# Kernel tuning notes

Measured on AMD Instinct MI355X. Metric: run time of the kernel, lower is better.

The kernel has to match this reference:

```python
import jax, jax.numpy as jnp
import numpy as np

N, M = 50000, 12
ORIG, NBR_F, AF = 92, 41, 64
B, NA = 500, 100
NCONV = 3
BN_EPS = 1e-5


def _batchnorm(x, g, b):
    # training-mode batchnorm over axis 0 (biased variance, like torch)
    mu = jnp.mean(x, axis=0)
    var = jnp.mean((x - mu) ** 2, axis=0)
    return (x - mu) * jax.lax.rsqrt(var + BN_EPS) * g + b


def _conv_layer(atom, nbr_fea, nbr_idx, W, bW, g1, b1, g2, b2):
    n, m = nbr_idx.shape
    atom_nbr = atom[nbr_idx]                                   # [N,M,AF] gather
    center = jnp.broadcast_to(atom[:, None, :], (n, m, AF))
    total = jnp.concatenate([center, atom_nbr, nbr_fea], axis=2)  # [N,M,2AF+NBR_F]
    gated = jnp.einsum('nmf,of->nmo', total, W) + bW              # [N,M,2AF]
    gated = _batchnorm(gated.reshape(-1, 2 * AF), g1, b1).reshape(n, m, 2 * AF)
    filt, core = gated[..., :AF], gated[..., AF:]
    summed = jnp.sum(jax.nn.sigmoid(filt) * jax.nn.softplus(core), axis=1)  # [N,AF]
    summed = _batchnorm(summed, g2, b2)
    return jax.nn.softplus(atom + summed)


def setup_inputs() -> dict:
    key = jax.random.key(0)
    ks = jax.random.split(key, 12)
    inp = {
        'atom_fea': jax.random.normal(ks[0], (N, ORIG), jnp.float32),
        'nbr_fea': jax.random.normal(ks[1], (N, M, NBR_F), jnp.float32),
        'nbr_fea_idx': jax.random.randint(ks[2], (N, M), 0, N, jnp.int32),
        'crystal_atom_idx': jnp.arange(B * NA, dtype=jnp.int32).reshape(B, NA),
        'mask': jnp.ones((ORIG,), jnp.float32),
        'emb_W': jax.random.normal(ks[3], (AF, ORIG), jnp.float32) * 0.05,
        'conv_W': jax.random.normal(ks[4], (NCONV, 2 * AF, 2 * AF + NBR_F), jnp.float32) * 0.05,
        'conv_b': jnp.zeros((NCONV, 2 * AF), jnp.float32),
        'bn1_g': jnp.ones((NCONV, 2 * AF), jnp.float32),
        'bn1_b': jnp.zeros((NCONV, 2 * AF), jnp.float32),
        'bn2_g': jnp.ones((NCONV, AF), jnp.float32),
        'bn2_b': jnp.zeros((NCONV, AF), jnp.float32),
        'fc1_W': jax.random.normal(ks[5], (AF, AF), jnp.float32) * 0.05,
        'fc1_b': jnp.zeros((AF,), jnp.float32),
        'fc2_W': jax.random.normal(ks[6], (AF, AF), jnp.float32) * 0.05,
        'fc2_b': jnp.zeros((AF,), jnp.float32),
        'out_W': jax.random.normal(ks[7], (1, AF), jnp.float32) * 0.05,
        'out_b': jnp.zeros((1,), jnp.float32),
    }
    return inp


def reference(atom_fea, nbr_fea, nbr_fea_idx, crystal_atom_idx, mask, emb_W,
              conv_W, conv_b, bn1_g, bn1_b, bn2_g, bn2_b,
              fc1_W, fc1_b, fc2_W, fc2_b, out_W, out_b):
    x = atom_fea * mask                      # learned input mask
    atom_mask_feature = x
    h = x @ emb_W.T                          # embedding, no bias -> [N,AF]
    for i in range(NCONV):
        h = _conv_layer(h, nbr_fea, nbr_fea_idx, conv_W[i], conv_b[i],
                        bn1_g[i], bn1_b[i], bn2_g[i], bn2_b[i])
    g = h[crystal_atom_idx]                  # [B,NA,AF]
    norm = jnp.sqrt(jnp.sum(g * g, axis=-1, keepdims=True))
    g = g / jnp.maximum(norm, 1e-12)         # F.normalize p=2
    pooled = jnp.mean(g, axis=1)             # [B,AF]
    z = jax.nn.softplus(pooled @ fc1_W.T + fc1_b)
    z = jax.nn.softplus(z @ fc2_W.T + fc2_b)
    props = z @ out_W.T + out_b              # [B,1]
    return props, atom_mask_feature
```

## Files before the change

kernel.cpp:

```cpp
#include <hip/hip_runtime.h>
#include <hip/hip_bf16.h>
#include <stdint.h>

#define NN      50000
#define MMN     12
#define NMROWS  600000
#define ORIGF   92
#define NBRF    41
#define AFD     64
#define GCH     128
#define KTOT    169
#define BBC     500
#define NAA     100
#define BN_EPS  1e-5f
#define GROWS   96

typedef unsigned short u16;
typedef __attribute__((ext_vector_type(8))) short bf16x8;
typedef __attribute__((ext_vector_type(4))) float f32x4;
typedef __attribute__((ext_vector_type(4))) unsigned int u32x4;

__device__ __forceinline__ float b2f(u16 u) {
    union { uint32_t i; float f; } v; v.i = ((uint32_t)u) << 16; return v.f;
}
__device__ __forceinline__ float hi2f(uint32_t p) {
    union { uint32_t i; float f; } v; v.i = p & 0xffff0000u; return v.f;
}
__device__ __forceinline__ u16 f2b(float f) {
    __hip_bfloat16 h = __float2bfloat16(f);
    return *(u16*)&h;
}
__device__ __forceinline__ float sp_f(float x) {
    return fmaxf(x, 0.f) + __logf(1.f + __expf(-fabsf(x)));
}
__device__ __forceinline__ float sigm_f(float x) {
    return __builtin_amdgcn_rcpf(1.f + __expf(-x));
}

__global__ void k_mask(const float* __restrict__ atom, const float* __restrict__ mask,
                       float* __restrict__ dout) {
    int i = blockIdx.x * blockDim.x + threadIdx.x;
    int stride = gridDim.x * blockDim.x;
    for (; i < NN * ORIGF; i += stride) {
        int k = i % ORIGF;
        dout[BBC + i] = atom[i] * mask[k];
    }
}

__global__ __launch_bounds__(256, 2) void k_emb(const float* __restrict__ atom,
                                                const float* __restrict__ mask,
                                                const float* __restrict__ embW,
                                                u16* __restrict__ h) {
    __shared__ float xs[4 * 96];
    int lane = threadIdx.x & 63;
    int w = threadIdx.x >> 6;
    float wr[ORIGF];
#pragma unroll
    for (int k = 0; k < ORIGF; ++k) wr[k] = embW[lane * ORIGF + k];
    float m1 = mask[lane];
    float m2 = (lane < ORIGF - 64) ? mask[64 + lane] : 0.f;
    for (int base = blockIdx.x * 4; base < NN; base += gridDim.x * 4) {
        int n = base + w;
        xs[w * 96 + lane] = atom[(size_t)n * ORIGF + lane] * m1;
        if (lane < ORIGF - 64)
            xs[w * 96 + 64 + lane] = atom[(size_t)n * ORIGF + 64 + lane] * m2;
        __syncthreads();
        float acc = 0.f;
#pragma unroll
        for (int k4 = 0; k4 < ORIGF / 4; ++k4) {
            float4 f = *(const float4*)&xs[w * 96 + 4 * k4];
            acc += f.x * wr[4*k4] + f.y * wr[4*k4+1] + f.z * wr[4*k4+2] + f.w * wr[4*k4+3];
        }
        h[(size_t)n * AFD + lane] = f2b(acc);
        __syncthreads();
    }
}

__global__ __launch_bounds__(256, 2) void k_cn(const u16* __restrict__ h,
                                               const float* __restrict__ convW,
                                               uint32_t* __restrict__ C32) {
    __shared__ float xs[2 * AFD];
    int lane = threadIdx.x & 63;
    int w = threadIdx.x >> 6;
    int half = w & 1;
    int sub = w >> 1;
    int koff = half * AFD;
    float wa[AFD], wb[AFD];
#pragma unroll
    for (int k = 0; k < AFD; ++k) {
        wa[k] = convW[lane * KTOT + koff + k];
        wb[k] = convW[(lane + 64) * KTOT + koff + k];
    }
    for (int base = blockIdx.x * 2; base < NN; base += gridDim.x * 2) {
        int n = base + sub;
        if (half == 0) xs[sub * AFD + lane] = b2f(h[(size_t)n * AFD + lane]);
        __syncthreads();
        float aa = 0.f, ab = 0.f;
#pragma unroll
        for (int k4 = 0; k4 < AFD / 4; ++k4) {
            float4 f = *(const float4*)&xs[sub * AFD + 4 * k4];
            aa += f.x * wa[4*k4] + f.y * wa[4*k4+1] + f.z * wa[4*k4+2] + f.w * wa[4*k4+3];
            ab += f.x * wb[4*k4] + f.y * wb[4*k4+1] + f.z * wb[4*k4+2] + f.w * wb[4*k4+3];
        }
        C32[(size_t)n * 128 + half * 64 + lane] = (uint32_t)f2b(aa) | ((uint32_t)f2b(ab) << 16);
        __syncthreads();
    }
}

__device__ __forceinline__ void stage_nbrf(const float* nbrf, int r0, float* fs) {
    const float4* src = (const float4*)(nbrf + (size_t)r0 * NBRF);
    for (int t = threadIdx.x; t < (GROWS * NBRF) / 4; t += 256) {
        float4 f = src[t];
        float vals[4] = {f.x, f.y, f.z, f.w};
#pragma unroll
        for (int j = 0; j < 4; ++j) {
            int e = t * 4 + j;
            int row = e / NBRF;
            int k = e - row * NBRF;
            fs[row * 44 + k] = vals[j];
        }
    }
}

template<bool STORE>
__global__ __launch_bounds__(256, 4) void k_gs5(
    const uint32_t* __restrict__ C32, const float* __restrict__ nbrf,
    const int* __restrict__ nbridx, const float* __restrict__ convW,
    const float* __restrict__ convb, float* __restrict__ stats,
    uint32_t* __restrict__ gated32)
{
    __shared__ __align__(16) u16 As[GROWS * 48];
    __shared__ __align__(16) uint32_t C2T[64 * 100];
    __shared__ __align__(16) uint32_t C1T[64 * 12];
    const int tid  = threadIdx.x;
    const int lane = tid & 63;
    const int w    = tid >> 6;
    const int lr   = lane & 15;
    const int lg   = lane >> 4;
    const int r0    = blockIdx.x * GROWS;
    const int nbase = blockIdx.x * (GROWS / MMN);
    const int rowb  = w * 24;

    int jv = nbridx[r0 + rowb + (lane < 24 ? lane : 0)];
    uint32_t c1v[2];
#pragma unroll
    for (int q = 0; q < 2; ++q) {
        int e = tid + q * 256;
        c1v[q] = C32[(size_t)(nbase + (e >> 6)) * 128 + (e & 63)];
    }
    const float4* src4 = (const float4*)(nbrf + (size_t)r0 * NBRF);
    float4 af[4];
#pragma unroll
    for (int it = 0; it < 4; ++it) {
        int t = tid + it * 256;
        if (it < 3 || t < 984) af[it] = src4[t];
    }
    const int chlo = w * 16 + lr;
    const int chhi = chlo + 64;
    const float* wlo = convW + (size_t)chlo * KTOT + 128;
    const float* whi = convW + (size_t)chhi * KTOT + 128;
    bf16x8 bl0, bh0;
    bf16x8 bl1 = {0,0,0,0,0,0,0,0}, bh1 = {0,0,0,0,0,0,0,0};
#pragma unroll
    for (int e = 0; e < 8; ++e) {
        bl0[e] = (short)f2b(wlo[8 * lg + e]);
        bh0[e] = (short)f2b(whi[8 * lg + e]);
    }
    if (lg == 0) {
#pragma unroll
        for (int e = 0; e < 8; ++e) {
            bl1[e] = (short)f2b(wlo[32 + e]);
            bh1[e] = (short)f2b(whi[32 + e]);
        }
    } else if (lg == 1) {
        bl1[0] = (short)f2b(wlo[40]); bl1[1] = (short)f2b(convb[chlo]);
        bh1[0] = (short)f2b(whi[40]); bh1[1] = (short)f2b(convb[chhi]);
    }
    uint32_t c2v[24];
#pragma unroll
    for (int rr = 0; rr < 24; ++rr) {
        int j = __shfl(jv, rr, 64);
        c2v[rr] = C32[(size_t)j * 128 + 64 + lane];
    }
#pragma unroll
    for (int it = 0; it < 4; ++it) {
        int t = tid + it * 256;
        if (it < 3 || t < 984) {
            float4 f = af[it];
            float vals[4] = {f.x, f.y, f.z, f.w};
#pragma unroll
            for (int jj = 0; jj < 4; ++jj) {
                int e = t * 4 + jj;
                int row = e / NBRF;
                int k = e - row * NBRF;
                As[row * 48 + k] = f2b(vals[jj]);
            }
        }
    }
    for (int e = tid; e < 672; e += 256) {
        int row = e / 7;
        int k = 41 + (e - row * 7);
        As[row * 48 + k] = (k == 41) ? (u16)0x3F80 : (u16)0;
    }
#pragma unroll
    for (int q = 0; q < 2; ++q) {
        int e = tid + q * 256;
        C1T[(e & 63) * 12 + (e >> 6)] = c1v[q];
    }
#pragma unroll
    for (int rr = 0; rr < 24; ++rr) C2T[lane * 100 + rowb + rr] = c2v[rr];
    __syncthreads();

    f32x4 acc[6][2];
    const f32x4 z = {0.f, 0.f, 0.f, 0.f};
    const bf16x8 zb = {0,0,0,0,0,0,0,0};
#pragma unroll
    for (int mt = 0; mt < 6; ++mt) {
        const u16* ap = &As[(mt * 16 + lr) * 48 + 8 * lg];
        bf16x8 a0 = *(const bf16x8*)ap;
        bf16x8 a1 = zb;
        if (lg < 2) a1 = *(const bf16x8*)(ap + 32);
        acc[mt][0] = __builtin_amdgcn_mfma_f32_16x16x32_bf16(a1, bl1,
                     __builtin_amdgcn_mfma_f32_16x16x32_bf16(a0, bl0, z, 0, 0, 0), 0, 0, 0);
        acc[mt][1] = __builtin_amdgcn_mfma_f32_16x16x32_bf16(a1, bh1,
                     __builtin_amdgcn_mfma_f32_16x16x32_bf16(a0, bh0, z, 0, 0, 0), 0, 0, 0);
    }

    const int word = w * 16 + lr;
    float slo = 0.f, qlo = 0.f, shi = 0.f, qhi = 0.f;
#pragma unroll
    for (int mt = 0; mt < 6; ++mt) {
        u32x4 p2 = *(const u32x4*)&C2T[word * 100 + mt * 16 + 4 * lg];
#pragma unroll
        for (int rg = 0; rg < 4; ++rg) {
            int row = mt * 16 + 4 * lg + rg;
            uint32_t p1 = C1T[word * 12 + row / MMN];
            float glo = acc[mt][0][rg] + b2f((u16)p1) + b2f((u16)p2[rg]);
            float ghi = acc[mt][1][rg] + hi2f(p1) + hi2f(p2[rg]);
            if (STORE) {
                gated32[(size_t)(r0 + row) * 64 + word] =
                    (uint32_t)f2b(glo) | ((uint32_t)f2b(ghi) << 16);
            }
            slo += glo; qlo = fmaf(glo, glo, qlo);
            shi += ghi; qhi = fmaf(ghi, ghi, qhi);
        }
    }
    slo += __shfl_xor(slo, 16, 64); slo += __shfl_xor(slo, 32, 64);
    qlo += __shfl_xor(qlo, 16, 64); qlo += __shfl_xor(qlo, 32, 64);
    shi += __shfl_xor(shi, 16, 64); shi += __shfl_xor(shi, 32, 64);
    qhi += __shfl_xor(qhi, 16, 64); qhi += __shfl_xor(qhi, 32, 64);
    if (lane < 16) {
        atomicAdd(&stats[word], slo);
        atomicAdd(&stats[128 + word], qlo);
        atomicAdd(&stats[64 + word], shi);
        atomicAdd(&stats[128 + 64 + word], qhi);
    }
}

__global__ void k_fin(float* __restrict__ stats, const float* __restrict__ gg,
                      const float* __restrict__ bb, int nch, float invcnt,
                      int sumoff, int sqoff, int scoff, int shoff) {
    int c = threadIdx.x;
    if (c < nch) {
        float mean = stats[sumoff + c] * invcnt;
        float var  = fmaxf(stats[sqoff + c] * invcnt - mean * mean, 0.f);
        float sc   = gg[c] * rsqrtf(var + BN_EPS);
        stats[scoff + c] = sc;
        stats[shoff + c] = bb[c] - mean * sc;
    }
}

__global__ __launch_bounds__(256) void k_acts(
    const uint32_t* __restrict__ gated32, float* __restrict__ stats,
    u16* __restrict__ summed)
{
    __shared__ float red[4][64][2];
    int lane = threadIdx.x & 63;
    int w = threadIdx.x >> 6;
    float sa = stats[384 + lane],      ba = stats[512 + lane];
    float sb = stats[384 + 64 + lane], bb = stats[512 + 64 + lane];
    int wave = blockIdx.x * 4 + w, nw = gridDim.x * 4;
    float s2 = 0.f, q2 = 0.f;
    for (int n = wave; n < NN; n += nw) {
        const uint32_t* gr = gated32 + (size_t)n * MMN * 64;
        float s = 0.f;
#pragma unroll
        for (int m = 0; m < MMN; ++m) {
            uint32_t p = gr[m * 64 + lane];
            float f1 = b2f((u16)p) * sa + ba;
            float cc = hi2f(p) * sb + bb;
            s += sigm_f(f1) * sp_f(cc);
        }
        summed[(size_t)n * AFD + lane] = f2b(s);
        s2 += s; q2 += s * s;
    }
    red[w][lane][0] = s2; red[w][lane][1] = q2;
    __syncthreads();
    if (threadIdx.x < 64) {
        int c = threadIdx.x;
        float a = 0, b = 0;
#pragma unroll
        for (int ww = 0; ww < 4; ++ww) { a += red[ww][c][0]; b += red[ww][c][1]; }
        atomicAdd(&stats[256 + c], a);
        atomicAdd(&stats[320 + c], b);
    }
}

__device__ __forceinline__ void edge_dot(const float* fr, const float* wfa,
                                         const float* wfb, float& aa, float& ab) {
#pragma unroll
    for (int k4 = 0; k4 < 10; ++k4) {
        float4 f = *(const float4*)&fr[4 * k4];
        aa += f.x * wfa[4*k4] + f.y * wfa[4*k4+1] + f.z * wfa[4*k4+2] + f.w * wfa[4*k4+3];
        ab += f.x * wfb[4*k4] + f.y * wfb[4*k4+1] + f.z * wfb[4*k4+2] + f.w * wfb[4*k4+3];
    }
    aa += fr[40] * wfa[40];
    ab += fr[40] * wfb[40];
}

__global__ __launch_bounds__(256) void k_act(
    const uint32_t* __restrict__ C32, const float* __restrict__ nbrf,
    const int* __restrict__ nbridx, const float* __restrict__ convW,
    const float* __restrict__ convb, float* __restrict__ stats,
    u16* __restrict__ summed)
{
    __shared__ float fs[GROWS * 44];
    __shared__ float red[4][64][2];
    int lane = threadIdx.x & 63;
    int w = threadIdx.x >> 6;
    int r0 = blockIdx.x * GROWS;
    stage_nbrf(nbrf, r0, fs);
    float wfa[NBRF], wfb[NBRF];
#pragma unroll
    for (int k = 0; k < NBRF; ++k) {
        wfa[k] = convW[lane * KTOT + 128 + k];
        wfb[k] = convW[(lane + 64) * KTOT + 128 + k];
    }
    float biasa = convb[lane], biasb = convb[64 + lane];
    float sa = stats[384 + lane],      ba = stats[512 + lane];
    float sb = stats[384 + 64 + lane], bb = stats[512 + 64 + lane];
    __syncthreads();
    float s2 = 0.f, q2 = 0.f;
    float s = 0.f;
    float c1a = 0.f, c1b = 0.f;
    for (int rr = 0; rr < 24; ++rr) {
        int rl = w * 24 + rr;
        int r = r0 + rl;
        if ((rr % MMN) == 0) {
            int n = r / MMN;
            uint32_t p1 = C32[(size_t)n * 128 + lane];
            c1a = b2f((u16)p1); c1b = b2f((u16)(p1 >> 16));
            s = 0.f;
        }
        int j = nbridx[r];
        uint32_t p2 = C32[(size_t)j * 128 + 64 + lane];
        float aa = c1a + b2f((u16)p2) + biasa;
        float ab = c1b + b2f((u16)(p2 >> 16)) + biasb;
        edge_dot(&fs[rl * 44], wfa, wfb, aa, ab);
        float f1 = aa * sa + ba;
        float cc = ab * sb + bb;
        s += sigm_f(f1) * sp_f(cc);
        if ((rr % MMN) == MMN - 1) {
            int n = r / MMN;
            summed[(size_t)n * AFD + lane] = f2b(s);
            s2 += s; q2 += s * s;
        }
    }
    red[w][lane][0] = s2; red[w][lane][1] = q2;
    __syncthreads();
    if (threadIdx.x < 64) {
        int c = threadIdx.x;
        float a = 0, b = 0;
#pragma unroll
        for (int ww = 0; ww < 4; ++ww) { a += red[ww][c][0]; b += red[ww][c][1]; }
        atomicAdd(&stats[256 + c], a);
        atomicAdd(&stats[320 + c], b);
    }
}

__global__ void k_update(u16* __restrict__ h, const u16* __restrict__ summed,
                         const float* __restrict__ stats) {
    int i = blockIdx.x * blockDim.x + threadIdx.x;
    int st = gridDim.x * blockDim.x;
    int c = threadIdx.x & 63;
    float sc = stats[640 + c], shf = stats[704 + c];
    for (; i < NN * AFD; i += st) {
        float x = b2f(h[i]) + b2f(summed[i]) * sc + shf;
        h[i] = f2b(sp_f(x));
    }
}

__global__ __launch_bounds__(256) void k_pool(const u16* __restrict__ h,
                                              const int* __restrict__ cry,
                                              float* __restrict__ pooled) {
    __shared__ float red[4][64];
    int lane = threadIdx.x & 63, w = threadIdx.x >> 6;
    int b = blockIdx.x;
    float acc = 0.f;
    for (int a = w; a < NAA; a += 4) {
        int idx = cry[b * NAA + a];
        float v = b2f(h[(size_t)idx * AFD + lane]);
        float s2 = v * v;
#pragma unroll
        for (int o = 32; o > 0; o >>= 1) s2 += __shfl_xor(s2, o, 64);
        acc += v / fmaxf(sqrtf(s2), 1e-12f);
    }
    red[w][lane] = acc;
    __syncthreads();
    if (threadIdx.x < 64) {
        float s = red[0][threadIdx.x] + red[1][threadIdx.x] +
                  red[2][threadIdx.x] + red[3][threadIdx.x];
        pooled[b * AFD + threadIdx.x] = s * (1.f / NAA);
    }
}

__global__ __launch_bounds__(64) void k_head(const float* __restrict__ pooled,
    const float* __restrict__ fc1W, const float* __restrict__ fc1b,
    const float* __restrict__ fc2W, const float* __restrict__ fc2b,
    const float* __restrict__ outW, const float* __restrict__ outb,
    float* __restrict__ props) {
    __shared__ float W1[64 * 65], W2[64 * 65], zbuf[64], pbuf[64];
    int l = threadIdx.x;
    for (int e = l; e < 64 * 64; e += 64) {
        int o = e >> 6, k = e & 63;
        W1[o * 65 + k] = fc1W[e];
        W2[o * 65 + k] = fc2W[e];
    }
    int b = blockIdx.x;
    pbuf[l] = pooled[b * AFD + l];
    __syncthreads();
    float acc = fc1b[l];
#pragma unroll
    for (int k = 0; k < 64; ++k) acc += pbuf[k] * W1[l * 65 + k];
    zbuf[l] = sp_f(acc);
    __syncthreads();
    acc = fc2b[l];
#pragma unroll
    for (int k = 0; k < 64; ++k) acc += zbuf[k] * W2[l * 65 + k];
    float v = sp_f(acc) * outW[l];
#pragma unroll
    for (int o = 32; o > 0; o >>= 1) v += __shfl_xor(v, o, 64);
    if (l == 0) props[b] = v + outb[0];
}

extern "C" void kernel_launch(void* const* d_in, const int* in_sizes, int n_in,
                              void* d_out, int out_size, void* d_ws, size_t ws_size,
                              hipStream_t stream) {
    const float* atom  = (const float*)d_in[0];
    const float* nbrf  = (const float*)d_in[1];
    const int* nbridx  = (const int*)d_in[2];
    const int* cry     = (const int*)d_in[3];
    const float* mask  = (const float*)d_in[4];
    const float* embW  = (const float*)d_in[5];
    const float* convW = (const float*)d_in[6];
    const float* convb = (const float*)d_in[7];
    const float* bn1g  = (const float*)d_in[8];
    const float* bn1b  = (const float*)d_in[9];
    const float* bn2g  = (const float*)d_in[10];
    const float* bn2b  = (const float*)d_in[11];
    const float* fc1W  = (const float*)d_in[12];
    const float* fc1b  = (const float*)d_in[13];
    const float* fc2W  = (const float*)d_in[14];
    const float* fc2b  = (const float*)d_in[15];
    const float* outW  = (const float*)d_in[16];
    const float* outb  = (const float*)d_in[17];

    char* ws = (char*)d_ws;
    float* stats    = (float*)ws;
    float* pooled   = (float*)(ws + 4096);
    u16*   h        = (u16*)(ws + (1u << 20));
    u16*   summed   = (u16*)(ws + (8u << 20));
    uint32_t* C32   = (uint32_t*)(ws + (16u << 20));
    uint32_t* gated32 = (uint32_t*)(ws + (48u << 20));
    const bool bigws = ws_size >= (size_t)(48u << 20) + 153600000u;

    float* out_props = (float*)d_out;

    k_mask<<<2048, 256, 0, stream>>>(atom, mask, (float*)d_out);
    k_emb<<<512, 256, 0, stream>>>(atom, mask, embW, h);
    for (int i = 0; i < 3; ++i) {
        hipMemsetAsync(stats, 0, 384 * sizeof(float), stream);
        k_cn<<<1024, 256, 0, stream>>>(h, convW + (size_t)i * GCH * KTOT, C32);
        if (bigws)
            k_gs5<true><<<NMROWS / GROWS, 256, 0, stream>>>(C32, nbrf, nbridx,
                convW + (size_t)i * GCH * KTOT, convb + (size_t)i * GCH, stats, gated32);
        else
            k_gs5<false><<<NMROWS / GROWS, 256, 0, stream>>>(C32, nbrf, nbridx,
                convW + (size_t)i * GCH * KTOT, convb + (size_t)i * GCH, stats, gated32);
        k_fin<<<1, 128, 0, stream>>>(stats, bn1g + (size_t)i * GCH, bn1b + (size_t)i * GCH,
                                     128, 1.f / NMROWS, 0, 128, 384, 512);
        if (bigws)
            k_acts<<<1024, 256, 0, stream>>>(gated32, stats, summed);
        else
            k_act<<<NMROWS / GROWS, 256, 0, stream>>>(C32, nbrf, nbridx,
                convW + (size_t)i * GCH * KTOT, convb + (size_t)i * GCH, stats, summed);
        k_fin<<<1, 128, 0, stream>>>(stats, bn2g + (size_t)i * AFD, bn2b + (size_t)i * AFD,
                                     64, 1.f / NN, 256, 320, 640, 704);
        k_update<<<1024, 256, 0, stream>>>(h, summed, stats);
    }
    k_pool<<<BBC, 256, 0, stream>>>(h, cry, pooled);
    k_head<<<BBC, 64, 0, stream>>>(pooled, fc1W, fc1b, fc2W, fc2b, outW, outb, out_props);
}
```

Baseline: 1.041 ms.

## Recompute gated tile in a second MFMA pass instead of storing gated buffer

Replaces the stats pass plus the separate activation kernel with one templated kernel run twice. The first pass only accumulates batchnorm statistics. The second recomputes the gated values with MFMA and applies sigmoid·softplus, reducing per-atom sums in shared memory. This drops the large gated32 write and read-back in exchange for redoing the gather and matmul. The neighbor gathers now go straight to LDS via global_load_lds, replacing register staging and the transposed LDS writes.

```diff
diff --git a/kernel.cpp b/kernel.cpp
--- a/kernel.cpp
+++ b/kernel.cpp
@@ -18,7 +18,6 @@
 typedef unsigned short u16;
 typedef __attribute__((ext_vector_type(8))) short bf16x8;
 typedef __attribute__((ext_vector_type(4))) float f32x4;
-typedef __attribute__((ext_vector_type(4))) unsigned int u32x4;
 
 __device__ __forceinline__ float b2f(u16 u) {
     union { uint32_t i; float f; } v; v.i = ((uint32_t)u) << 16; return v.f;
@@ -35,6 +34,11 @@
 }
 __device__ __forceinline__ float sigm_f(float x) {
     return __builtin_amdgcn_rcpf(1.f + __expf(-x));
+}
+__device__ __forceinline__ void gll4(const void* g, void* l) {
+    __builtin_amdgcn_global_load_lds(
+        (const __attribute__((address_space(1))) void*)g,
+        (__attribute__((address_space(3))) void*)l, 4, 0, 0);
 }
 
 __global__ void k_mask(const float* __restrict__ atom, const float* __restrict__ mask,
@@ -107,46 +111,37 @@
     }
 }
 
-__device__ __forceinline__ void stage_nbrf(const float* nbrf, int r0, float* fs) {
-    const float4* src = (const float4*)(nbrf + (size_t)r0 * NBRF);
-    for (int t = threadIdx.x; t < (GROWS * NBRF) / 4; t += 256) {
-        float4 f = src[t];
-        float vals[4] = {f.x, f.y, f.z, f.w};
-#pragma unroll
-        for (int j = 0; j < 4; ++j) {
-            int e = t * 4 + j;
-            int row = e / NBRF;
-            int k = e - row * NBRF;
-            fs[row * 44 + k] = vals[j];
-        }
-    }
-}
-
-template<bool STORE>
-__global__ __launch_bounds__(256, 4) void k_gs5(
+template<int PASS>
+__global__ __launch_bounds__(256, 4) void k_gs6(
     const uint32_t* __restrict__ C32, const float* __restrict__ nbrf,
     const int* __restrict__ nbridx, const float* __restrict__ convW,
     const float* __restrict__ convb, float* __restrict__ stats,
-    uint32_t* __restrict__ gated32)
+    u16* __restrict__ summed)
 {
     __shared__ __align__(16) u16 As[GROWS * 48];
-    __shared__ __align__(16) uint32_t C2T[64 * 100];
-    __shared__ __align__(16) uint32_t C1T[64 * 12];
+    __shared__ uint32_t C2s[GROWS * 64];
+    __shared__ uint32_t C1s[8 * 64];
+    __shared__ float sred[8 * 64];
     const int tid  = threadIdx.x;
     const int lane = tid & 63;
     const int w    = tid >> 6;
     const int lr   = lane & 15;
     const int lg   = lane >> 4;
     const int r0    = blockIdx.x * GROWS;
-    const int nbase = blockIdx.x * (GROWS / MMN);
-    const int rowb  = w * 24;
-
-    int jv = nbridx[r0 + rowb + (lane < 24 ? lane : 0)];
-    uint32_t c1v[2];
-#pragma unroll
-    for (int q = 0; q < 2; ++q) {
-        int e = tid + q * 256;
-        c1v[q] = C32[(size_t)(nbase + (e >> 6)) * 128 + (e & 63)];
+    const int nbase = blockIdx.x * 8;
+    const int wq   = __builtin_amdgcn_readfirstlane(w);
+    const int rowb = wq * 24;
+
+    {
+        int a0 = wq * 2;
+        gll4(&C32[(size_t)(nbase + a0) * 128 + lane],     &C1s[a0 * 64]);
+        gll4(&C32[(size_t)(nbase + a0 + 1) * 128 + lane], &C1s[(a0 + 1) * 64]);
+    }
+    const int* nb = nbridx + r0 + rowb;
+#pragma unroll
+    for (int rr = 0; rr < 24; ++rr) {
+        int j = nb[rr];
+        gll4(&C32[(size_t)j * 128 + 64 + lane], &C2s[(rowb + rr) * 64]);
     }
     const float4* src4 = (const float4*)(nbrf + (size_t)r0 * NBRF);
     float4 af[4];
@@ -176,11 +171,11 @@
         bl1[0] = (short)f2b(wlo[40]); bl1[1] = (short)f2b(convb[chlo]);
         bh1[0] = (short)f2b(whi[40]); bh1[1] = (short)f2b(convb[chhi]);
     }
-    uint32_t c2v[24];
-#pragma unroll
-    for (int rr = 0; rr < 24; ++rr) {
-        int j = __shfl(jv, rr, 64);
-        c2v[rr] = C32[(size_t)j * 128 + 64 + lane];
+    const int word = w * 16 + lr;
+    float sa = 0.f, ba = 0.f, sb = 0.f, bbv = 0.f;
+    if (PASS == 2) {
+        sa = stats[384 + word];      ba = stats[512 + word];
+        sb = stats[384 + 64 + word]; bbv = stats[512 + 64 + word];
     }
 #pragma unroll
     for (int it = 0; it < 4; ++it) {
@@ -202,13 +197,9 @@
         int k = 41 + (e - row * 7);
         As[row * 48 + k] = (k == 41) ? (u16)0x3F80 : (u16)0;
     }
-#pragma unroll
-    for (int q = 0; q < 2; ++q) {
-        int e = tid + q * 256;
-        C1T[(e & 63) * 12 + (e >> 6)] = c1v[q];
-    }
-#pragma unroll
-    for (int rr = 0; rr < 24; ++rr) C2T[lane * 100 + rowb + rr] = c2v[rr];
+    if (PASS == 2) {
+        sred[tid] = 0.f; sred[tid + 256] = 0.f;
+    }
     __syncthreads();
 
     f32x4 acc[6][2];
@@ -226,34 +217,59 @@
                      __builtin_amdgcn_mfma_f32_16x16x32_bf16(a0, bh0, z, 0, 0, 0), 0, 0, 0);
     }
 
-    const int word = w * 16 + lr;
-    float slo = 0.f, qlo = 0.f, shi = 0.f, qhi = 0.f;
-#pragma unroll
-    for (int mt = 0; mt < 6; ++mt) {
-        u32x4 p2 = *(const u32x4*)&C2T[word * 100 + mt * 16 + 4 * lg];
-#pragma unroll
-        for (int rg = 0; rg < 4; ++rg) {
-            int row = mt * 16 + 4 * lg + rg;
-            uint32_t p1 = C1T[word * 12 + row / MMN];
-            float glo = acc[mt][0][rg] + b2f((u16)p1) + b2f((u16)p2[rg]);
-            float ghi = acc[mt][1][rg] + hi2f(p1) + hi2f(p2[rg]);
-            if (STORE) {
-                gated32[(size_t)(r0 + row) * 64 + word] =
-                    (uint32_t)f2b(glo) | ((uint32_t)f2b(ghi) << 16);
+    if (PASS == 1) {
+        float slo = 0.f, qlo = 0.f, shi = 0.f, qhi = 0.f;
+#pragma unroll
+        for (int mt = 0; mt < 6; ++mt) {
+            int atom = (mt * 16 + 4 * lg) / 12;
+            uint32_t p1 = C1s[atom * 64 + word];
+            float c1lo = b2f((u16)p1), c1hi = hi2f(p1);
+#pragma unroll
+            for (int rg = 0; rg < 4; ++rg) {
+                int row = mt * 16 + 4 * lg + rg;
+                uint32_t p2 = C2s[row * 64 + word];
+                float glo = acc[mt][0][rg] + c1lo + b2f((u16)p2);
+                float ghi = acc[mt][1][rg] + c1hi + hi2f(p2);
+                slo += glo; qlo = fmaf(glo, glo, qlo);
+                shi += ghi; qhi = fmaf(ghi, ghi, qhi);
             }
-            slo += glo; qlo = fmaf(glo, glo, qlo);
-            shi += ghi; qhi = fmaf(ghi, ghi, qhi);
-        }
-    }
-    slo += __shfl_xor(slo, 16, 64); slo += __shfl_xor(slo, 32, 64);
-    qlo += __shfl_xor(qlo, 16, 64); qlo += __shfl_xor(qlo, 32, 64);
-    shi += __shfl_xor(shi, 16, 64); shi += __shfl_xor(shi, 32, 64);
-    qhi += __shfl_xor(qhi, 16, 64); qhi += __shfl_xor(qhi, 32, 64);
-    if (lane < 16) {
-        atomicAdd(&stats[word], slo);
-        atomicAdd(&stats[128 + word], qlo);
-        atomicAdd(&stats[64 + word], shi);
-        atomicAdd(&stats[128 + 64 + word], qhi);
+        }
+        slo += __shfl_xor(slo, 16, 64); slo += __shfl_xor(slo, 32, 64);
+        qlo += __shfl_xor(qlo, 16, 64); qlo += __shfl_xor(qlo, 32, 64);
+        shi += __shfl_xor(shi, 16, 64); shi += __shfl_xor(shi, 32, 64);
+        qhi += __shfl_xor(qhi, 16, 64); qhi += __shfl_xor(qhi, 32, 64);
+        if (lane < 16) {
+            atomicAdd(&stats[word], slo);
+            atomicAdd(&stats[128 + word], qlo);
+            atomicAdd(&stats[64 + word], shi);
+            atomicAdd(&stats[128 + 64 + word], qhi);
+        }
+    } else {
+#pragma unroll
+        for (int mt = 0; mt < 6; ++mt) {
+            int atom = (mt * 16 + 4 * lg) / 12;
+            uint32_t p1 = C1s[atom * 64 + word];
+            float c1lo = b2f((u16)p1), c1hi = hi2f(p1);
+            float pm = 0.f;
+#pragma unroll
+            for (int rg = 0; rg < 4; ++rg) {
+                int row = mt * 16 + 4 * lg + rg;
+                uint32_t p2 = C2s[row * 64 + word];
+                float glo = acc[mt][0][rg] + c1lo + b2f((u16)p2);
+                float ghi = acc[mt][1][rg] + c1hi + hi2f(p2);
+                pm += sigm_f(glo * sa + ba) * sp_f(ghi * sb + bbv);
+            }
+            atomicAdd(&sred[atom * 64 + word], pm);
+        }
+        __syncthreads();
+        int word2 = tid & 63;
+        int a = tid >> 6;
+        float v1 = sred[a * 64 + word2];
+        float v2 = sred[(a + 4) * 64 + word2];
+        summed[(size_t)(nbase + a) * AFD + word2] = f2b(v1);
+        summed[(size_t)(nbase + a + 4) * AFD + word2] = f2b(v2);
+        atomicAdd(&stats[256 + word2], v1 + v2);
+        atomicAdd(&stats[320 + word2], v1 * v1 + v2 * v2);
     }
 }
 
@@ -267,114 +283,6 @@
         float sc   = gg[c] * rsqrtf(var + BN_EPS);
         stats[scoff + c] = sc;
         stats[shoff + c] = bb[c] - mean * sc;
-    }
-}
-
-__global__ __launch_bounds__(256) void k_acts(
-    const uint32_t* __restrict__ gated32, float* __restrict__ stats,
-    u16* __restrict__ summed)
-{
-    __shared__ float red[4][64][2];
-    int lane = threadIdx.x & 63;
-    int w = threadIdx.x >> 6;
-    float sa = stats[384 + lane],      ba = stats[512 + lane];
-    float sb = stats[384 + 64 + lane], bb = stats[512 + 64 + lane];
-    int wave = blockIdx.x * 4 + w, nw = gridDim.x * 4;
-    float s2 = 0.f, q2 = 0.f;
-    for (int n = wave; n < NN; n += nw) {
-        const uint32_t* gr = gated32 + (size_t)n * MMN * 64;
-        float s = 0.f;
-#pragma unroll
-        for (int m = 0; m < MMN; ++m) {
-            uint32_t p = gr[m * 64 + lane];
-            float f1 = b2f((u16)p) * sa + ba;
-            float cc = hi2f(p) * sb + bb;
-            s += sigm_f(f1) * sp_f(cc);
-        }
-        summed[(size_t)n * AFD + lane] = f2b(s);
-        s2 += s; q2 += s * s;
-    }
-    red[w][lane][0] = s2; red[w][lane][1] = q2;
-    __syncthreads();
-    if (threadIdx.x < 64) {
-        int c = threadIdx.x;
-        float a = 0, b = 0;
-#pragma unroll
-        for (int ww = 0; ww < 4; ++ww) { a += red[ww][c][0]; b += red[ww][c][1]; }
-        atomicAdd(&stats[256 + c], a);
-        atomicAdd(&stats[320 + c], b);
-    }
-}
-
-__device__ __forceinline__ void edge_dot(const float* fr, const float* wfa,
-                                         const float* wfb, float& aa, float& ab) {
-#pragma unroll
-    for (int k4 = 0; k4 < 10; ++k4) {
-        float4 f = *(const float4*)&fr[4 * k4];
-        aa += f.x * wfa[4*k4] + f.y * wfa[4*k4+1] + f.z * wfa[4*k4+2] + f.w * wfa[4*k4+3];
-        ab += f.x * wfb[4*k4] + f.y * wfb[4*k4+1] + f.z * wfb[4*k4+2] + f.w * wfb[4*k4+3];
-    }
-    aa += fr[40] * wfa[40];
-    ab += fr[40] * wfb[40];
-}
-
-__global__ __launch_bounds__(256) void k_act(
-    const uint32_t* __restrict__ C32, const float* __restrict__ nbrf,
-    const int* __restrict__ nbridx, const float* __restrict__ convW,
-    const float* __restrict__ convb, float* __restrict__ stats,
-    u16* __restrict__ summed)
-{
-    __shared__ float fs[GROWS * 44];
-    __shared__ float red[4][64][2];
-    int lane = threadIdx.x & 63;
-    int w = threadIdx.x >> 6;
-    int r0 = blockIdx.x * GROWS;
-    stage_nbrf(nbrf, r0, fs);
-    float wfa[NBRF], wfb[NBRF];
-#pragma unroll
-    for (int k = 0; k < NBRF; ++k) {
-        wfa[k] = convW[lane * KTOT + 128 + k];
-        wfb[k] = convW[(lane + 64) * KTOT + 128 + k];
-    }
-    float biasa = convb[lane], biasb = convb[64 + lane];
-    float sa = stats[384 + lane],      ba = stats[512 + lane];
-    float sb = stats[384 + 64 + lane], bb = stats[512 + 64 + lane];
-    __syncthreads();
-    float s2 = 0.f, q2 = 0.f;
-    float s = 0.f;
-    float c1a = 0.f, c1b = 0.f;
-    for (int rr = 0; rr < 24; ++rr) {
-        int rl = w * 24 + rr;
-        int r = r0 + rl;
-        if ((rr % MMN) == 0) {
-            int n = r / MMN;
-            uint32_t p1 = C32[(size_t)n * 128 + lane];
-            c1a = b2f((u16)p1); c1b = b2f((u16)(p1 >> 16));
-            s = 0.f;
-        }
-        int j = nbridx[r];
-        uint32_t p2 = C32[(size_t)j * 128 + 64 + lane];
-        float aa = c1a + b2f((u16)p2) + biasa;
-        float ab = c1b + b2f((u16)(p2 >> 16)) + biasb;
-        edge_dot(&fs[rl * 44], wfa, wfb, aa, ab);
-        float f1 = aa * sa + ba;
-        float cc = ab * sb + bb;
-        s += sigm_f(f1) * sp_f(cc);
-        if ((rr % MMN) == MMN - 1) {
-            int n = r / MMN;
-            summed[(size_t)n * AFD + lane] = f2b(s);
-            s2 += s; q2 += s * s;
-        }
-    }
-    red[w][lane][0] = s2; red[w][lane][1] = q2;
-    __syncthreads();
-    if (threadIdx.x < 64) {
-        int c = threadIdx.x;
-        float a = 0, b = 0;
-#pragma unroll
-        for (int ww = 0; ww < 4; ++ww) { a += red[ww][c][0]; b += red[ww][c][1]; }
-        atomicAdd(&stats[256 + c], a);
-        atomicAdd(&stats[320 + c], b);
     }
 }
 
@@ -471,8 +379,6 @@
     u16*   h        = (u16*)(ws + (1u << 20));
     u16*   summed   = (u16*)(ws + (8u << 20));
     uint32_t* C32   = (uint32_t*)(ws + (16u << 20));
-    uint32_t* gated32 = (uint32_t*)(ws + (48u << 20));
-    const bool bigws = ws_size >= (size_t)(48u << 20) + 153600000u;
 
     float* out_props = (float*)d_out;
 
@@ -481,19 +387,12 @@
     for (int i = 0; i < 3; ++i) {
         hipMemsetAsync(stats, 0, 384 * sizeof(float), stream);
         k_cn<<<1024, 256, 0, stream>>>(h, convW + (size_t)i * GCH * KTOT, C32);
-        if (bigws)
-            k_gs5<true><<<NMROWS / GROWS, 256, 0, stream>>>(C32, nbrf, nbridx,
-                convW + (size_t)i * GCH * KTOT, convb + (size_t)i * GCH, stats, gated32);
-        else
-            k_gs5<false><<<NMROWS / GROWS, 256, 0, stream>>>(C32, nbrf, nbridx,
-                convW + (size_t)i * GCH * KTOT, convb + (size_t)i * GCH, stats, gated32);
+        k_gs6<1><<<NMROWS / GROWS, 256, 0, stream>>>(C32, nbrf, nbridx,
+            convW + (size_t)i * GCH * KTOT, convb + (size_t)i * GCH, stats, summed);
         k_fin<<<1, 128, 0, stream>>>(stats, bn1g + (size_t)i * GCH, bn1b + (size_t)i * GCH,
                                      128, 1.f / NMROWS, 0, 128, 384, 512);
-        if (bigws)
-            k_acts<<<1024, 256, 0, stream>>>(gated32, stats, summed);
-        else
-            k_act<<<NMROWS / GROWS, 256, 0, stream>>>(C32, nbrf, nbridx,
-                convW + (size_t)i * GCH * KTOT, convb + (size_t)i * GCH, stats, summed);
+        k_gs6<2><<<NMROWS / GROWS, 256, 0, stream>>>(C32, nbrf, nbridx,
+            convW + (size_t)i * GCH * KTOT, convb + (size_t)i * GCH, stats, summed);
         k_fin<<<1, 128, 0, stream>>>(stats, bn2g + (size_t)i * AFD, bn2b + (size_t)i * AFD,
                                      64, 1.f / NN, 256, 320, 640, 704);
         k_update<<<1024, 256, 0, stream>>>(h, summed, stats);
```

New measurement: 2.757 ms. +164.9%, slower.

## Halve gather-GEMM tile to 48 rows, raise occupancy, re-layout shared staging

Applied to the files above, without the earlier changes.

The gather-GEMM kernel now handles 48 edge rows per block instead of 96 and raises the launch-bounds occupancy target from 4 to 8 blocks per CU. Each wave loads its 12 neighbour indices directly instead of shuffling them. The C1/C2 shared buffers move to a row-major padded layout, so stores and epilogue reads use per-row scalar loads rather than transposed vector loads. The aim is more concurrent waves to hide gather latency, at the cost of twice as many blocks, more per-block weight setup and twice as many stats atomics. The activation kernel grid is also doubled.

```diff
diff --git a/kernel.cpp b/kernel.cpp
--- a/kernel.cpp
+++ b/kernel.cpp
@@ -14,11 +14,11 @@
 #define NAA     100
 #define BN_EPS  1e-5f
 #define GROWS   96
+#define G48     48
 
 typedef unsigned short u16;
 typedef __attribute__((ext_vector_type(8))) short bf16x8;
 typedef __attribute__((ext_vector_type(4))) float f32x4;
-typedef __attribute__((ext_vector_type(4))) unsigned int u32x4;
 
 __device__ __forceinline__ float b2f(u16 u) {
     union { uint32_t i; float f; } v; v.i = ((uint32_t)u) << 16; return v.f;
@@ -123,37 +123,39 @@
 }
 
 template<bool STORE>
-__global__ __launch_bounds__(256, 4) void k_gs5(
+__global__ __launch_bounds__(256, 8) void k_gs9(
     const uint32_t* __restrict__ C32, const float* __restrict__ nbrf,
     const int* __restrict__ nbridx, const float* __restrict__ convW,
     const float* __restrict__ convb, float* __restrict__ stats,
     uint32_t* __restrict__ gated32)
 {
-    __shared__ __align__(16) u16 As[GROWS * 48];
-    __shared__ __align__(16) uint32_t C2T[64 * 100];
-    __shared__ __align__(16) uint32_t C1T[64 * 12];
+    __shared__ __align__(16) u16 As[G48 * 48];
+    __shared__ uint32_t C2s[G48 * 68];
+    __shared__ uint32_t C1s[4 * 68];
     const int tid  = threadIdx.x;
     const int lane = tid & 63;
     const int w    = tid >> 6;
     const int lr   = lane & 15;
     const int lg   = lane >> 4;
-    const int r0    = blockIdx.x * GROWS;
-    const int nbase = blockIdx.x * (GROWS / MMN);
-    const int rowb  = w * 24;
-
-    int jv = nbridx[r0 + rowb + (lane < 24 ? lane : 0)];
-    uint32_t c1v[2];
-#pragma unroll
-    for (int q = 0; q < 2; ++q) {
-        int e = tid + q * 256;
-        c1v[q] = C32[(size_t)(nbase + (e >> 6)) * 128 + (e & 63)];
+    const int r0    = blockIdx.x * G48;
+    const int nbase = blockIdx.x * 4;
+    const int wq   = __builtin_amdgcn_readfirstlane(w);
+    const int rowb = wq * 12;
+
+    uint32_t c1v = C32[(size_t)(nbase + (tid >> 6)) * 128 + (tid & 63)];
+    const int* nb = nbridx + r0 + rowb;
+    uint32_t c2v[12];
+#pragma unroll
+    for (int rr = 0; rr < 12; ++rr) {
+        int j = nb[rr];
+        c2v[rr] = C32[(size_t)j * 128 + 64 + lane];
     }
     const float4* src4 = (const float4*)(nbrf + (size_t)r0 * NBRF);
-    float4 af[4];
-#pragma unroll
-    for (int it = 0; it < 4; ++it) {
+    float4 af[2];
+#pragma unroll
+    for (int it = 0; it < 2; ++it) {
         int t = tid + it * 256;
-        if (it < 3 || t < 984) af[it] = src4[t];
+        if (it == 0 || t < 492) af[it] = src4[t];
     }
     const int chlo = w * 16 + lr;
     const int chhi = chlo + 64;
@@ -176,16 +178,10 @@
         bl1[0] = (short)f2b(wlo[40]); bl1[1] = (short)f2b(convb[chlo]);
         bh1[0] = (short)f2b(whi[40]); bh1[1] = (short)f2b(convb[chhi]);
     }
-    uint32_t c2v[24];
-#pragma unroll
-    for (int rr = 0; rr < 24; ++rr) {
-        int j = __shfl(jv, rr, 64);
-        c2v[rr] = C32[(size_t)j * 128 + 64 + lane];
-    }
-#pragma unroll
-    for (int it = 0; it < 4; ++it) {
+#pragma unroll
+    for (int it = 0; it < 2; ++it) {
         int t = tid + it * 256;
-        if (it < 3 || t < 984) {
+        if (it == 0 || t < 492) {
             float4 f = af[it];
             float vals[4] = {f.x, f.y, f.z, f.w};
 #pragma unroll
@@ -197,25 +193,21 @@
             }
         }
     }
-    for (int e = tid; e < 672; e += 256) {
+    for (int e = tid; e < 336; e += 256) {
         int row = e / 7;
         int k = 41 + (e - row * 7);
         As[row * 48 + k] = (k == 41) ? (u16)0x3F80 : (u16)0;
     }
-#pragma unroll
-    for (int q = 0; q < 2; ++q) {
-        int e = tid + q * 256;
-        C1T[(e & 63) * 12 + (e >> 6)] = c1v[q];
-    }
-#pragma unroll
-    for (int rr = 0; rr < 24; ++rr) C2T[lane * 100 + rowb + rr] = c2v[rr];
-    __syncthreads();
-
-    f32x4 acc[6][2];
+    C1s[(tid >> 6) * 68 + (tid & 63)] = c1v;
+#pragma unroll
+    for (int rr = 0; rr < 12; ++rr) C2s[(rowb + rr) * 68 + lane] = c2v[rr];
+    __syncthreads();
+
+    f32x4 acc[3][2];
     const f32x4 z = {0.f, 0.f, 0.f, 0.f};
     const bf16x8 zb = {0,0,0,0,0,0,0,0};
 #pragma unroll
-    for (int mt = 0; mt < 6; ++mt) {
+    for (int mt = 0; mt < 3; ++mt) {
         const u16* ap = &As[(mt * 16 + lr) * 48 + 8 * lg];
         bf16x8 a0 = *(const bf16x8*)ap;
         bf16x8 a1 = zb;
@@ -229,14 +221,16 @@
     const int word = w * 16 + lr;
     float slo = 0.f, qlo = 0.f, shi = 0.f, qhi = 0.f;
 #pragma unroll
-    for (int mt = 0; mt < 6; ++mt) {
-        u32x4 p2 = *(const u32x4*)&C2T[word * 100 + mt * 16 + 4 * lg];
+    for (int mt = 0; mt < 3; ++mt) {
+        int atomi = (mt * 16 + 4 * lg) / 12;
+        uint32_t p1 = C1s[atomi * 68 + word];
+        float c1lo = b2f((u16)p1), c1hi = hi2f(p1);
 #pragma unroll
         for (int rg = 0; rg < 4; ++rg) {
             int row = mt * 16 + 4 * lg + rg;
-            uint32_t p1 = C1T[word * 12 + row / MMN];
-            float glo = acc[mt][0][rg] + b2f((u16)p1) + b2f((u16)p2[rg]);
-            float ghi = acc[mt][1][rg] + hi2f(p1) + hi2f(p2[rg]);
+            uint32_t p2 = C2s[row * 68 + word];
+            float glo = acc[mt][0][rg] + c1lo + b2f((u16)p2);
+            float ghi = acc[mt][1][rg] + c1hi + hi2f(p2);
             if (STORE) {
                 gated32[(size_t)(r0 + row) * 64 + word] =
                     (uint32_t)f2b(glo) | ((uint32_t)f2b(ghi) << 16);
@@ -482,15 +476,15 @@
         hipMemsetAsync(stats, 0, 384 * sizeof(float), stream);
         k_cn<<<1024, 256, 0, stream>>>(h, convW + (size_t)i * GCH * KTOT, C32);
         if (bigws)
-            k_gs5<true><<<NMROWS / GROWS, 256, 0, stream>>>(C32, nbrf, nbridx,
+            k_gs9<true><<<NMROWS / G48, 256, 0, stream>>>(C32, nbrf, nbridx,
                 convW + (size_t)i * GCH * KTOT, convb + (size_t)i * GCH, stats, gated32);
         else
-            k_gs5<false><<<NMROWS / GROWS, 256, 0, stream>>>(C32, nbrf, nbridx,
+            k_gs9<false><<<NMROWS / G48, 256, 0, stream>>>(C32, nbrf, nbridx,
                 convW + (size_t)i * GCH * KTOT, convb + (size_t)i * GCH, stats, gated32);
         k_fin<<<1, 128, 0, stream>>>(stats, bn1g + (size_t)i * GCH, bn1b + (size_t)i * GCH,
                                      128, 1.f / NMROWS, 0, 128, 384, 512);
         if (bigws)
-            k_acts<<<1024, 256, 0, stream>>>(gated32, stats, summed);
+            k_acts<<<2048, 256, 0, stream>>>(gated32, stats, summed);
         else
             k_act<<<NMROWS / GROWS, 256, 0, stream>>>(C32, nbrf, nbridx,
                 convW + (size_t)i * GCH * KTOT, convb + (size_t)i * GCH, stats, summed);
```

Measured after the change: 1.540 ms. +48.0%, slower.
